# Optimization experiments

Hardware: AMD Instinct MI355X
Metric: run time of the kernel (lower is better)

The kernel has to match this reference:

```python
import jax, jax.numpy as jnp
import numpy as np

EMB = 1024
NUM_HEADS = 16
HEAD_DIM = EMB // NUM_HEADS
ROPE_BASE = 10000.0


def rotate_half(x):
    # Non-standard interleaved rotate: out[..., 2i] = -x[..., 2i+1], out[..., 2i+1] = x[..., 2i]
    x1 = x[..., ::2]
    x2 = x[..., 1::2]
    return jnp.stack((-x2, x1), axis=-1).reshape(x.shape)


def rope_cos_sin(seq_len, start_pos=0):
    inv_freq = 1.0 / (ROPE_BASE ** (jnp.arange(0, HEAD_DIM, 2, dtype=jnp.float32) / HEAD_DIM))
    positions = jnp.arange(start_pos, start_pos + seq_len, dtype=jnp.float32)
    freqs = jnp.outer(positions, inv_freq)           # [S, HEAD_DIM/2]
    emb = jnp.concatenate([freqs, freqs], axis=-1)   # [S, HEAD_DIM]
    return jnp.cos(emb)[None, None], jnp.sin(emb)[None, None]  # [1,1,S,D]


def setup_inputs() -> dict:
    key = jax.random.key(0)
    k1, k2, k3 = jax.random.split(key, 3)
    x = jax.random.normal(k1, (1, 2048, EMB), dtype=jnp.float32)
    Wqkv = jax.random.normal(k2, (3 * EMB, EMB), dtype=jnp.float32) * 0.02
    Wout = jax.random.normal(k3, (EMB, EMB), dtype=jnp.float32) * 0.02
    return {"x": x, "Wqkv": Wqkv, "Wout": Wout}


def reference(x, Wqkv, Wout):
    batch, seq_len, _ = x.shape
    qkv = jnp.einsum('bse,fe->bsf', x, Wqkv)                      # [B,S,3E]
    qkv = qkv.reshape(batch, seq_len, 3, NUM_HEADS, HEAD_DIM)
    qkv = jnp.transpose(qkv, (2, 0, 3, 1, 4))                     # [3,B,H,S,D]
    q, k, v = qkv[0], qkv[1], qkv[2]

    cos, sin = rope_cos_sin(seq_len, start_pos=0)
    q = q * cos + rotate_half(q) * sin
    cos_k, sin_k = rope_cos_sin(seq_len, start_pos=0)
    k = k * cos_k + rotate_half(k) * sin_k

    # causal scaled dot-product attention
    scale = 1.0 / jnp.sqrt(jnp.float32(HEAD_DIM))
    scores = jnp.einsum('bhqd,bhkd->bhqk', q, k) * scale          # [B,H,S,S]
    causal = jnp.tril(jnp.ones((seq_len, seq_len), dtype=bool))
    scores = jnp.where(causal[None, None], scores, jnp.finfo(scores.dtype).min)
    attn = jax.nn.softmax(scores, axis=-1)
    out = jnp.einsum('bhqk,bhkd->bhqd', attn, v)                  # [B,H,S,D]

    out = jnp.transpose(out, (0, 2, 1, 3)).reshape(batch, seq_len, EMB)
    return jnp.einsum('bse,fe->bsf', out, Wout)
```

## Files before the change

### kernel.cpp

```cpp
#include <hip/hip_runtime.h>

#define DEVI __device__ __forceinline__

typedef __bf16 bf16x8 __attribute__((ext_vector_type(8)));
typedef float  f32x4  __attribute__((ext_vector_type(4)));
typedef unsigned short u16;

static DEVI u16 f2bf(float f){
  unsigned u = __builtin_bit_cast(unsigned, f);
  u += 0x7fffu + ((u >> 16) & 1u);
  return (u16)(u >> 16);
}

static DEVI f32x4 mfma16(bf16x8 a, bf16x8 b, f32x4 c){
  return __builtin_amdgcn_mfma_f32_16x16x32_bf16(a, b, c, 0, 0, 0);
}

static DEVI void gload_lds16(const void* g, void* l){
  __builtin_amdgcn_global_load_lds((const __attribute__((address_space(1))) unsigned int*)g,
                                   (__attribute__((address_space(3))) unsigned int*)l,
                                   16, 0, 0);
}

__global__ void convert_kernel(const float* __restrict__ x, const float* __restrict__ wq,
                               const float* __restrict__ wo,
                               u16* __restrict__ xb, u16* __restrict__ wqb, u16* __restrict__ wob){
  const int NX = 2048*1024, NQ = 3072*1024, NW = 1024*1024;
  const int total4 = (NX + NQ + NW) / 4;
  for (int i = blockIdx.x*blockDim.x + threadIdx.x; i < total4; i += gridDim.x*blockDim.x){
    int e = i * 4;
    const float* src; u16* dst; int off;
    if (e < NX)           { src = x;  dst = xb;  off = e; }
    else if (e < NX + NQ) { src = wq; dst = wqb; off = e - NX; }
    else                  { src = wo; dst = wob; off = e - NX - NQ; }
    float4 v = *(const float4*)(src + off);
    ushort4 o;
    o.x = f2bf(v.x); o.y = f2bf(v.y); o.z = f2bf(v.z); o.w = f2bf(v.w);
    *(ushort4*)(dst + off) = o;
  }
}

template<int EPI>
__global__ __launch_bounds__(512, 1)
void gemm_bt(const u16* __restrict__ A, const u16* __restrict__ B, int K,
             float* __restrict__ C, int ldc,
             u16* __restrict__ v_t, float* __restrict__ qkf){
  __shared__ u16 As[128*64];
  __shared__ u16 Bs[128*64];
  const int tid  = threadIdx.x;
  const int lane = tid & 63;
  const int wid  = tid >> 6;
  const int wr   = wid >> 2, wc = wid & 3;
  const int l15  = lane & 15, lg = lane >> 4;
  const int bm   = blockIdx.y * 128, bn = blockIdx.x * 128;

  const int c0 = tid, c1 = tid + 512;
  const int r0 = c0 >> 3, r1 = c1 >> 3;
  const int gb0 = ((c0 & 7) << 4) ^ ((r0 & 7) << 4);
  const int gb1 = ((c1 & 7) << 4) ^ ((r1 & 7) << 4);
  const u16* Ag0 = A + (size_t)(bm + r0) * K + (gb0 >> 1);
  const u16* Ag1 = A + (size_t)(bm + r1) * K + (gb1 >> 1);
  const u16* Bg0 = B + (size_t)(bn + r0) * K + (gb0 >> 1);
  const u16* Bg1 = B + (size_t)(bn + r1) * K + (gb1 >> 1);

  int baseA[4], swzA[4], baseB[2], swzB[2];
  #pragma unroll
  for (int m = 0; m < 4; ++m){
    int r = wr*64 + m*16 + l15;
    baseA[m] = r * 128; swzA[m] = (r & 7) << 4;
  }
  #pragma unroll
  for (int n = 0; n < 2; ++n){
    int r = wc*32 + n*16 + l15;
    baseB[n] = r * 128; swzB[n] = (r & 7) << 4;
  }
  const int colb = lg * 16;

  f32x4 acc[4][2] = {};
  const char* Ab = (const char*)As;
  const char* Bb = (const char*)Bs;

  for (int kb = 0; kb < K; kb += 64){
    gload_lds16(Ag0 + kb, &As[c0 * 8]);
    gload_lds16(Ag1 + kb, &As[c1 * 8]);
    gload_lds16(Bg0 + kb, &Bs[c0 * 8]);
    gload_lds16(Bg1 + kb, &Bs[c1 * 8]);
    __syncthreads();
    #pragma unroll
    for (int kk = 0; kk < 2; ++kk){
      bf16x8 av[4], bv[2];
      #pragma unroll
      for (int m = 0; m < 4; ++m)
        av[m] = *(const bf16x8*)(Ab + baseA[m] + ((kk*64 + colb) ^ swzA[m]));
      #pragma unroll
      for (int n = 0; n < 2; ++n)
        bv[n] = *(const bf16x8*)(Bb + baseB[n] + ((kk*64 + colb) ^ swzB[n]));
      #pragma unroll
      for (int m = 0; m < 4; ++m)
        #pragma unroll
        for (int n = 0; n < 2; ++n)
          acc[m][n] = mfma16(av[m], bv[n], acc[m][n]);
    }
    __syncthreads();
  }

  #pragma unroll
  for (int m = 0; m < 4; ++m){
    const int srow = bm + wr*64 + m*16 + lg*4;
    #pragma unroll
    for (int n = 0; n < 2; ++n){
      const int f = bn + wc*32 + n*16 + l15;
      f32x4 v = acc[m][n];
      if (EPI == 0){
        #pragma unroll
        for (int r = 0; r < 4; ++r)
          C[(size_t)(srow + r)*ldc + f] = v[r];
      } else {
        const int which = f >> 10, rem = f & 1023;
        const int h = rem >> 6, d = rem & 63;
        if (which == 2){
          ushort4 p;
          p.x = f2bf(v[0]); p.y = f2bf(v[1]); p.z = f2bf(v[2]); p.w = f2bf(v[3]);
          *(ushort4*)(v_t + ((size_t)(h*64 + d))*2048 + srow) = p;
        } else {
          float* dst = qkf + (((size_t)(which*16 + h))*2048 + srow)*64 + d;
          #pragma unroll
          for (int r = 0; r < 4; ++r) dst[(size_t)r * 64] = v[r];
        }
      }
    }
  }
}

__global__ void rope_kernel(const float* __restrict__ qkf,
                            u16* __restrict__ q_r, u16* __restrict__ k_r){
  const int t = blockIdx.x*blockDim.x + threadIdx.x;
  const int i = t & 31;
  const int s = (t >> 5) & 2047;
  const int h = (t >> 16) & 15;
  const int w = t >> 20;
  const float2 xv = *(const float2*)(qkf + (((size_t)w*16 + h)*2048 + s)*64 + 2*i);
  const int idx0 = (2*i) & 31;
  const float NEGL = -0.41524101186091903f;
  const float f0 = exp2f(NEGL * (float)idx0);
  const float f1 = exp2f(NEGL * (float)(idx0 + 1));
  const float a0 = (float)s * f0, a1 = (float)s * f1;
  float s0, c0, s1, c1;
  sincosf(a0, &s0, &c0);
  sincosf(a1, &s1, &c1);
  const float o0 = xv.x * c0 - xv.y * s0;
  const float o1 = xv.y * c1 + xv.x * s1;
  u16* dst = (w == 0 ? q_r : k_r) + ((size_t)h*2048 + s)*64 + 2*i;
  ushort2 pr; pr.x = f2bf(o0); pr.y = f2bf(o1);
  *(ushort2*)dst = pr;
}

static DEVI void stage_kv(const u16* __restrict__ kg, const u16* __restrict__ vg,
                          u16* Ks, u16* Vs, int tid){
  #pragma unroll
  for (int i = 0; i < 2; ++i){
    const int c = tid + i*256;
    const int row = c >> 3;
    const int cb = ((c & 7) << 4) ^ ((row & 7) << 4);
    gload_lds16(kg + (size_t)row*64   + (cb >> 1), Ks + c*8);
    gload_lds16(vg + (size_t)row*2048 + (cb >> 1), Vs + c*8);
  }
}

__global__ __launch_bounds__(256)
void attn_kernel(const u16* __restrict__ q_r, const u16* __restrict__ k_r,
                 const u16* __restrict__ v_t, u16* __restrict__ ao){
  __shared__ u16 Ks[2][64*64];
  __shared__ u16 Vs[2][64*64];
  __shared__ u16 P[4][16*64];
  const int tid  = threadIdx.x;
  const int lane = tid & 63, w = tid >> 6;
  const int l15  = lane & 15, lg = lane >> 4;
  const int h    = blockIdx.y;
  const int tile = (int)gridDim.x - 1 - (int)blockIdx.x;
  const int q0   = tile * 64;
  const int qb   = q0 + w*16;
  const int nt   = tile + 1;

  const u16* kg = k_r + (size_t)h*2048*64;
  const u16* vg = v_t + (size_t)h*64*2048;

  bf16x8 qf[2];
  #pragma unroll
  for (int kk = 0; kk < 2; ++kk)
    qf[kk] = *(const bf16x8*)(q_r + ((size_t)h*2048 + qb + l15)*64 + kk*32 + lg*8);

  f32x4 o[4] = {};
  float m[4], l[4];
  #pragma unroll
  for (int r = 0; r < 4; ++r){ m[r] = -3.0e38f; l[r] = 0.f; }

  stage_kv(kg, vg, &Ks[0][0], &Vs[0][0], tid);
  asm volatile("s_waitcnt vmcnt(0)" ::: "memory");
  __syncthreads();

  int cur = 0;
  for (int ib = 0; ib < nt; ++ib){
    const int kb = ib * 64;
    if (ib + 1 < nt)
      stage_kv(kg + (size_t)(kb + 64)*64, vg + (kb + 64), &Ks[cur^1][0], &Vs[cur^1][0], tid);

    f32x4 s[4] = {};
    const char* Kb = (const char*)&Ks[cur][0];
    #pragma unroll
    for (int ct = 0; ct < 4; ++ct){
      const int row = ct*16 + l15;
      const int swz = (row & 7) << 4;
      #pragma unroll
      for (int kk = 0; kk < 2; ++kk){
        bf16x8 kf = *(const bf16x8*)(Kb + row*128 + ((kk*64 + lg*16) ^ swz));
        s[ct] = mfma16(qf[kk], kf, s[ct]);
      }
    }
    const bool maskb = (kb + 63 > qb);
    #pragma unroll
    for (int ct = 0; ct < 4; ++ct){
      const int key = kb + ct*16 + l15;
      #pragma unroll
      for (int r = 0; r < 4; ++r){
        float sv = s[ct][r] * 0.125f;
        if (maskb && key > (qb + lg*4 + r)) sv = -3.0e38f;
        s[ct][r] = sv;
      }
    }
    float sc[4];
    #pragma unroll
    for (int r = 0; r < 4; ++r){
      float v = fmaxf(fmaxf(s[0][r], s[1][r]), fmaxf(s[2][r], s[3][r]));
      #pragma unroll
      for (int off = 1; off < 16; off <<= 1) v = fmaxf(v, __shfl_xor(v, off));
      const float mn = fmaxf(m[r], v);
      sc[r] = __expf(m[r] - mn);
      m[r] = mn;
    }
    float rs[4] = {0.f, 0.f, 0.f, 0.f};
    #pragma unroll
    for (int ct = 0; ct < 4; ++ct)
      #pragma unroll
      for (int r = 0; r < 4; ++r){
        const float p = __expf(s[ct][r] - m[r]);
        s[ct][r] = p;
        rs[r] += p;
      }
    #pragma unroll
    for (int r = 0; r < 4; ++r){
      float v = rs[r];
      #pragma unroll
      for (int off = 1; off < 16; off <<= 1) v += __shfl_xor(v, off);
      l[r] = l[r]*sc[r] + v;
    }
    #pragma unroll
    for (int dt = 0; dt < 4; ++dt)
      #pragma unroll
      for (int r = 0; r < 4; ++r) o[dt][r] *= sc[r];

    char* Pb = (char*)&P[w][0];
    #pragma unroll
    for (int ct = 0; ct < 4; ++ct)
      #pragma unroll
      for (int r = 0; r < 4; ++r){
        const int row = lg*4 + r;
        const int cb  = (ct*32 + l15*2) ^ ((row & 7) << 4);
        *(u16*)(Pb + row*128 + cb) = f2bf(s[ct][r]);
      }
    asm volatile("s_waitcnt lgkmcnt(0)" ::: "memory");
    bf16x8 pf[2];
    {
      const int swzp = (l15 & 7) << 4;
      #pragma unroll
      for (int kk = 0; kk < 2; ++kk)
        pf[kk] = *(const bf16x8*)(Pb + l15*128 + ((kk*64 + lg*16) ^ swzp));
    }
    const char* Vb = (const char*)&Vs[cur][0];
    #pragma unroll
    for (int dt = 0; dt < 4; ++dt){
      const int d = dt*16 + l15;
      const int swz = (d & 7) << 4;
      #pragma unroll
      for (int kk = 0; kk < 2; ++kk){
        bf16x8 vf = *(const bf16x8*)(Vb + d*128 + ((kk*64 + lg*16) ^ swz));
        o[dt] = mfma16(pf[kk], vf, o[dt]);
      }
    }
    if (ib + 1 < nt){
      asm volatile("s_waitcnt vmcnt(0)" ::: "memory");
      __syncthreads();
      cur ^= 1;
    }
  }

  float inv[4];
  #pragma unroll
  for (int r = 0; r < 4; ++r) inv[r] = 1.0f / l[r];
  #pragma unroll
  for (int dt = 0; dt < 4; ++dt)
    #pragma unroll
    for (int r = 0; r < 4; ++r)
      ao[(size_t)(qb + lg*4 + r)*1024 + h*64 + dt*16 + l15] = f2bf(o[dt][r] * inv[r]);
}

extern "C" void kernel_launch(void* const* d_in, const int* in_sizes, int n_in,
                              void* d_out, int out_size, void* d_ws, size_t ws_size,
                              hipStream_t stream) {
  const float* x  = (const float*)d_in[0];
  const float* wq = (const float*)d_in[1];
  const float* wo = (const float*)d_in[2];
  float* out = (float*)d_out;

  char* w = (char*)d_ws;
  u16*   xb  = (u16*)(w + (size_t) 0);
  u16*   wqb = (u16*)(w + (size_t)( 4<<20));
  u16*   wob = (u16*)(w + (size_t)(10<<20));
  u16*   q_r = (u16*)(w + (size_t)(12<<20));
  u16*   k_r = (u16*)(w + (size_t)(16<<20));
  u16*   v_t = (u16*)(w + (size_t)(20<<20));
  u16*   ao  = (u16*)(w + (size_t)(24<<20));
  float* qkf = (float*)(w + (size_t)(28<<20));

  convert_kernel<<<2048, 256, 0, stream>>>(x, wq, wo, xb, wqb, wob);
  gemm_bt<1><<<dim3(24, 16), 512, 0, stream>>>(xb, wqb, 1024, nullptr, 0, v_t, qkf);
  rope_kernel<<<8192, 256, 0, stream>>>(qkf, q_r, k_r);
  attn_kernel<<<dim3(32, 16), 256, 0, stream>>>(q_r, k_r, v_t, ao);
  gemm_bt<0><<<dim3(8, 16), 512, 0, stream>>>(ao, wob, 1024, out, 1024, nullptr, nullptr);
}
```

Before: 189.3 us.

## Use 128-key attention tiles, XCD-aware head mapping, and defer row-sum reduction

The attention kernel now processes 128 keys per iteration instead of 64, which halves the number of loop iterations, barriers and softmax rescales, at the cost of doubled LDS for K/V/P and more registers. Blocks are remapped from a 1D grid so that each head's tiles land on the same XCD, which should improve L2 reuse of K/V. The per-iteration cross-lane row-sum shuffle is removed; lanes keep partial sums and reduce them once at the end. The added LDS and register pressure may lower occupancy.

```diff
diff --git a/kernel.cpp b/kernel.cpp
--- a/kernel.cpp
+++ b/kernel.cpp
@@ -155,32 +155,36 @@
   *(ushort2*)dst = pr;
 }
 
-static DEVI void stage_kv(const u16* __restrict__ kg, const u16* __restrict__ vg,
-                          u16* Ks, u16* Vs, int tid){
-  #pragma unroll
-  for (int i = 0; i < 2; ++i){
+static DEVI void stage_kv128(const u16* __restrict__ kg, const u16* __restrict__ vg,
+                             u16* Ks, u16* Vs, int tid){
+  #pragma unroll
+  for (int i = 0; i < 4; ++i){
     const int c = tid + i*256;
-    const int row = c >> 3;
-    const int cb = ((c & 7) << 4) ^ ((row & 7) << 4);
-    gload_lds16(kg + (size_t)row*64   + (cb >> 1), Ks + c*8);
-    gload_lds16(vg + (size_t)row*2048 + (cb >> 1), Vs + c*8);
+    const int kr = c >> 3;
+    const int kc = ((c & 7) << 4) ^ ((kr & 7) << 4);
+    gload_lds16(kg + (size_t)kr*64 + (kc >> 1), Ks + c*8);
+    const int vr = c >> 4;
+    const int vc = ((c & 15) << 4) ^ ((vr & 7) << 4);
+    gload_lds16(vg + (size_t)vr*2048 + (vc >> 1), Vs + c*8);
   }
 }
 
 __global__ __launch_bounds__(256)
 void attn_kernel(const u16* __restrict__ q_r, const u16* __restrict__ k_r,
                  const u16* __restrict__ v_t, u16* __restrict__ ao){
-  __shared__ u16 Ks[2][64*64];
-  __shared__ u16 Vs[2][64*64];
-  __shared__ u16 P[4][16*64];
+  __shared__ u16 Ks[2][128*64];
+  __shared__ u16 Vs[2][64*128];
+  __shared__ u16 P[4][16*128];
   const int tid  = threadIdx.x;
   const int lane = tid & 63, w = tid >> 6;
   const int l15  = lane & 15, lg = lane >> 4;
-  const int h    = blockIdx.y;
-  const int tile = (int)gridDim.x - 1 - (int)blockIdx.x;
+  const int bid  = blockIdx.x;
+  const int xcd  = bid & 7, j = bid >> 3;
+  const int h    = xcd + ((j >= 32) ? 8 : 0);
+  const int tile = 31 - (j & 31);
   const int q0   = tile * 64;
   const int qb   = q0 + w*16;
-  const int nt   = tile + 1;
+  const int nt   = (tile >> 1) + 1;
 
   const u16* kg = k_r + (size_t)h*2048*64;
   const u16* vg = v_t + (size_t)h*64*2048;
@@ -195,20 +199,21 @@
   #pragma unroll
   for (int r = 0; r < 4; ++r){ m[r] = -3.0e38f; l[r] = 0.f; }
 
-  stage_kv(kg, vg, &Ks[0][0], &Vs[0][0], tid);
+  stage_kv128(kg, vg, &Ks[0][0], &Vs[0][0], tid);
   asm volatile("s_waitcnt vmcnt(0)" ::: "memory");
   __syncthreads();
 
   int cur = 0;
   for (int ib = 0; ib < nt; ++ib){
-    const int kb = ib * 64;
+    const int kb = ib * 128;
     if (ib + 1 < nt)
-      stage_kv(kg + (size_t)(kb + 64)*64, vg + (kb + 64), &Ks[cur^1][0], &Vs[cur^1][0], tid);
-
-    f32x4 s[4] = {};
+      stage_kv128(kg + (size_t)(kb + 128)*64, vg + (kb + 128), &Ks[cur^1][0], &Vs[cur^1][0], tid);
+
+    f32x4 s[8];
     const char* Kb = (const char*)&Ks[cur][0];
     #pragma unroll
-    for (int ct = 0; ct < 4; ++ct){
+    for (int ct = 0; ct < 8; ++ct){
+      s[ct] = f32x4{0.f, 0.f, 0.f, 0.f};
       const int row = ct*16 + l15;
       const int swz = (row & 7) << 4;
       #pragma unroll
@@ -217,9 +222,9 @@
         s[ct] = mfma16(qf[kk], kf, s[ct]);
       }
     }
-    const bool maskb = (kb + 63 > qb);
-    #pragma unroll
-    for (int ct = 0; ct < 4; ++ct){
+    const bool maskb = (kb + 127 > qb);
+    #pragma unroll
+    for (int ct = 0; ct < 8; ++ct){
       const int key = kb + ct*16 + l15;
       #pragma unroll
       for (int r = 0; r < 4; ++r){
@@ -231,7 +236,9 @@
     float sc[4];
     #pragma unroll
     for (int r = 0; r < 4; ++r){
-      float v = fmaxf(fmaxf(s[0][r], s[1][r]), fmaxf(s[2][r], s[3][r]));
+      float v = s[0][r];
+      #pragma unroll
+      for (int ct = 1; ct < 8; ++ct) v = fmaxf(v, s[ct][r]);
       #pragma unroll
       for (int off = 1; off < 16; off <<= 1) v = fmaxf(v, __shfl_xor(v, off));
       const float mn = fmaxf(m[r], v);
@@ -240,7 +247,7 @@
     }
     float rs[4] = {0.f, 0.f, 0.f, 0.f};
     #pragma unroll
-    for (int ct = 0; ct < 4; ++ct)
+    for (int ct = 0; ct < 8; ++ct)
       #pragma unroll
       for (int r = 0; r < 4; ++r){
         const float p = __expf(s[ct][r] - m[r]);
@@ -248,12 +255,7 @@
         rs[r] += p;
       }
     #pragma unroll
-    for (int r = 0; r < 4; ++r){
-      float v = rs[r];
-      #pragma unroll
-      for (int off = 1; off < 16; off <<= 1) v += __shfl_xor(v, off);
-      l[r] = l[r]*sc[r] + v;
-    }
+    for (int r = 0; r < 4; ++r) l[r] = l[r]*sc[r] + rs[r];
     #pragma unroll
     for (int dt = 0; dt < 4; ++dt)
       #pragma unroll
@@ -261,20 +263,20 @@
 
     char* Pb = (char*)&P[w][0];
     #pragma unroll
-    for (int ct = 0; ct < 4; ++ct)
+    for (int ct = 0; ct < 8; ++ct)
       #pragma unroll
       for (int r = 0; r < 4; ++r){
         const int row = lg*4 + r;
         const int cb  = (ct*32 + l15*2) ^ ((row & 7) << 4);
-        *(u16*)(Pb + row*128 + cb) = f2bf(s[ct][r]);
+        *(u16*)(Pb + row*256 + cb) = f2bf(s[ct][r]);
       }
     asm volatile("s_waitcnt lgkmcnt(0)" ::: "memory");
-    bf16x8 pf[2];
+    bf16x8 pf[4];
     {
       const int swzp = (l15 & 7) << 4;
       #pragma unroll
-      for (int kk = 0; kk < 2; ++kk)
-        pf[kk] = *(const bf16x8*)(Pb + l15*128 + ((kk*64 + lg*16) ^ swzp));
+      for (int kk = 0; kk < 4; ++kk)
+        pf[kk] = *(const bf16x8*)(Pb + l15*256 + ((kk*64 + lg*16) ^ swzp));
     }
     const char* Vb = (const char*)&Vs[cur][0];
     #pragma unroll
@@ -282,8 +284,8 @@
       const int d = dt*16 + l15;
       const int swz = (d & 7) << 4;
       #pragma unroll
-      for (int kk = 0; kk < 2; ++kk){
-        bf16x8 vf = *(const bf16x8*)(Vb + d*128 + ((kk*64 + lg*16) ^ swz));
+      for (int kk = 0; kk < 4; ++kk){
+        bf16x8 vf = *(const bf16x8*)(Vb + d*256 + ((kk*64 + lg*16) ^ swz));
         o[dt] = mfma16(pf[kk], vf, o[dt]);
       }
     }
@@ -296,7 +298,12 @@
 
   float inv[4];
   #pragma unroll
-  for (int r = 0; r < 4; ++r) inv[r] = 1.0f / l[r];
+  for (int r = 0; r < 4; ++r){
+    float v = l[r];
+    #pragma unroll
+    for (int off = 1; off < 16; off <<= 1) v += __shfl_xor(v, off);
+    inv[r] = 1.0f / v;
+  }
   #pragma unroll
   for (int dt = 0; dt < 4; ++dt)
     #pragma unroll
@@ -325,6 +332,6 @@
   convert_kernel<<<2048, 256, 0, stream>>>(x, wq, wo, xb, wqb, wob);
   gemm_bt<1><<<dim3(24, 16), 512, 0, stream>>>(xb, wqb, 1024, nullptr, 0, v_t, qkf);
   rope_kernel<<<8192, 256, 0, stream>>>(qkf, q_r, k_r);
-  attn_kernel<<<dim3(32, 16), 256, 0, stream>>>(q_r, k_r, v_t, ao);
+  attn_kernel<<<512, 256, 0, stream>>>(q_r, k_r, v_t, ao);
   gemm_bt<0><<<dim3(8, 16), 512, 0, stream>>>(ao, wob, 1024, out, 1024, nullptr, nullptr);
 }
```

New measurement: 169.5 us. 1.12x faster.
